# Kernel tuning notes

Hardware: AMD Instinct MI355X
Metric: run time of the kernel (lower is better)

Reference implementation:

```python
import jax, jax.numpy as jnp
import numpy as np

HID = 1024
HEADS = 16
HEAD_DIM = HID // HEADS
FFN = 4096
EPS = 1e-5


def setup_inputs() -> dict:
    key = jax.random.key(0)
    ks = jax.random.split(key, 12)
    s = lambda k, shape, fan_in: jax.random.normal(k, shape, jnp.float32) * (fan_in ** -0.5)
    return {
        "hidden_states": jax.random.normal(ks[0], (2, 2048, HID), jnp.float32),
        "Wq": s(ks[1], (HID, HID), HID),
        "Wk": s(ks[2], (HID, HID), HID),
        "Wv": s(ks[3], (HID, HID), HID),
        "Wo": s(ks[4], (HID, HID), HID),
        "W1": s(ks[5], (HID, FFN), HID),
        "b1": jnp.zeros((FFN,), jnp.float32),
        "W2": s(ks[6], (FFN, HID), FFN),
        "b2": jnp.zeros((HID,), jnp.float32),
        "ln1_scale": jnp.ones((HID,), jnp.float32),
        "ln1_shift": jnp.zeros((HID,), jnp.float32),
        "ln2_scale": jnp.ones((HID,), jnp.float32),
        "ln2_shift": jnp.zeros((HID,), jnp.float32),
    }


def _layer_norm(x, scale, shift):
    mean = jnp.mean(x, axis=-1, keepdims=True)
    var = jnp.var(x, axis=-1, keepdims=True)  # biased, matches unbiased=False
    return (x - mean) * jax.lax.rsqrt(var + EPS) * scale + shift


def _forward(hidden_states, Wq, Wk, Wv, Wo, W1, b1, W2, b2,
             ln1_scale, ln1_shift, ln2_scale, ln2_shift):
    bsz, seq_len, _ = hidden_states.shape
    residual = hidden_states
    x = _layer_norm(hidden_states, ln1_scale, ln1_shift)

    # q/k/v projections -> [b, h, s, d]
    def proj(W):
        return (x @ W).reshape(bsz, seq_len, HEADS, HEAD_DIM).transpose(0, 2, 1, 3)
    q, k, v = proj(Wq), proj(Wk), proj(Wv)

    scores = jnp.einsum("bhqd,bhkd->bhqk", q, k)
    causal = jnp.triu(jnp.ones((seq_len, seq_len), bool), k=1)
    scores = jnp.where(causal, -jnp.inf, scores) / (HEAD_DIM ** 0.5)
    attn = jax.nn.softmax(scores, axis=-1)  # dropout is identity in eval
    out = jnp.einsum("bhqk,bhkd->bhqd", attn, v)
    out = out.transpose(0, 2, 1, 3).reshape(bsz, seq_len, HID)
    hidden_states = residual + out @ Wo

    residual = hidden_states
    y = _layer_norm(hidden_states, ln2_scale, ln2_shift)
    y = jax.nn.gelu(y @ W1 + b1, approximate=False) @ W2 + b2  # torch nn.GELU default = exact erf
    return residual + y


def reference(hidden_states, Wq, Wk, Wv, Wo, W1, b1, W2, b2,
              ln1_scale, ln1_shift, ln2_scale, ln2_shift):
    return _forward(hidden_states, Wq, Wk, Wv, Wo, W1, b1, W2, b2,
                    ln1_scale, ln1_shift, ln2_scale, ln2_shift)
```

## Files before the change

kernel.cpp:

```cpp
#include <hip/hip_runtime.h>
#include <math.h>

using bf16x8 = __attribute__((ext_vector_type(8))) short;
using f32x4  = __attribute__((ext_vector_type(4))) float;

struct __align__(8) us4 { unsigned short x, y, z, w; };
struct __align__(8) u32x2 { unsigned int x, y; };

__device__ __forceinline__ unsigned short f2b(float f) {
  union { float f; unsigned u; } v; v.f = f;
  unsigned r = v.u + 0x7FFFu + ((v.u >> 16) & 1u);
  return (unsigned short)(r >> 16);
}
__device__ __forceinline__ unsigned int cvt_pk_bf16(float lo, float hi) {
  unsigned int d;
  asm("v_cvt_pk_bf16_f32 %0, %1, %2" : "=v"(d) : "v"(lo), "v"(hi));
  return d;
}

#define GLDS(g, l) __builtin_amdgcn_global_load_lds(                        \
    (const __attribute__((address_space(1))) void*)(g),                    \
    (__attribute__((address_space(3))) void*)(l), 16, 0, 0)

__global__ void __launch_bounds__(256) prep_kernel(
    const float* __restrict__ hs, const float* __restrict__ ln1s,
    const float* __restrict__ ln1b, unsigned short* __restrict__ xb,
    const float* __restrict__ Wq, const float* __restrict__ Wk,
    const float* __restrict__ Wv, const float* __restrict__ Wo,
    const float* __restrict__ W1, const float* __restrict__ W2,
    unsigned short* __restrict__ wqkvT, unsigned short* __restrict__ woT,
    unsigned short* __restrict__ w1T, unsigned short* __restrict__ w2T) {
  const int id = blockIdx.x;
  const int t = threadIdx.x;
  __shared__ float tile[32][33];
  __shared__ float red[8];

  if (id < 4096) {
    const int row = id;
    const float4 v = ((const float4*)(hs + (size_t)row * 1024))[t];
    float s  = v.x + v.y + v.z + v.w;
    float s2 = v.x * v.x + v.y * v.y + v.z * v.z + v.w * v.w;
#pragma unroll
    for (int off = 32; off; off >>= 1) {
      s  += __shfl_xor(s,  off);
      s2 += __shfl_xor(s2, off);
    }
    const int w = t >> 6, lane = t & 63;
    if (!lane) { red[w] = s; red[4 + w] = s2; }
    __syncthreads();
    s  = red[0] + red[1] + red[2] + red[3];
    s2 = red[4] + red[5] + red[6] + red[7];
    const float mean = s * (1.0f / 1024.0f);
    const float var  = s2 * (1.0f / 1024.0f) - mean * mean;
    const float rstd = rsqrtf(var + 1e-5f);
    const float4 sc = ((const float4*)ln1s)[t];
    const float4 sh = ((const float4*)ln1b)[t];
    us4 o;
    o.x = f2b((v.x - mean) * rstd * sc.x + sh.x);
    o.y = f2b((v.y - mean) * rstd * sc.y + sh.y);
    o.z = f2b((v.z - mean) * rstd * sc.z + sh.z);
    o.w = f2b((v.w - mean) * rstd * sc.w + sh.w);
    ((us4*)(xb + (size_t)row * 1024))[t] = o;
    return;
  }

  const float* src; unsigned short* dst; int K, N, n0, k0;
  if (id < 8192) {
    const int which = (id - 4096) >> 10, local = (id - 4096) & 1023;
    src = (which == 0) ? Wq : (which == 1) ? Wk : (which == 2) ? Wv : Wo;
    dst = (which == 3) ? woT : wqkvT + (size_t)which * 1048576;
    K = 1024; N = 1024;
    n0 = (local & 31) * 32; k0 = (local >> 5) * 32;
  } else if (id < 12288) {
    const int local = id - 8192;
    src = W1; dst = w1T; K = 1024; N = 4096;
    n0 = (local & 127) * 32; k0 = (local >> 7) * 32;
  } else {
    const int local = id - 12288;
    src = W2; dst = w2T; K = 4096; N = 1024;
    n0 = (local & 31) * 32; k0 = (local >> 5) * 32;
  }
  const int tx = t & 31, ty = t >> 5;
#pragma unroll
  for (int i = 0; i < 32; i += 8)
    tile[ty + i][tx] = src[(size_t)(k0 + ty + i) * N + n0 + tx];
  __syncthreads();
#pragma unroll
  for (int i = 0; i < 32; i += 8)
    dst[(size_t)(n0 + ty + i) * K + k0 + tx] = f2b(tile[tx][ty + i]);
}

__global__ void __launch_bounds__(256) ln_kernel(
    const float* __restrict__ in, const float* __restrict__ scale,
    const float* __restrict__ shift, unsigned short* __restrict__ out) {
  const int row = blockIdx.x, t = threadIdx.x;
  const float4 v = ((const float4*)(in + (size_t)row * 1024))[t];
  float s  = v.x + v.y + v.z + v.w;
  float s2 = v.x * v.x + v.y * v.y + v.z * v.z + v.w * v.w;
#pragma unroll
  for (int off = 32; off; off >>= 1) {
    s  += __shfl_xor(s,  off);
    s2 += __shfl_xor(s2, off);
  }
  __shared__ float red[8];
  const int w = t >> 6, lane = t & 63;
  if (!lane) { red[w] = s; red[4 + w] = s2; }
  __syncthreads();
  s  = red[0] + red[1] + red[2] + red[3];
  s2 = red[4] + red[5] + red[6] + red[7];
  const float mean = s * (1.0f / 1024.0f);
  const float var  = s2 * (1.0f / 1024.0f) - mean * mean;
  const float rstd = rsqrtf(var + 1e-5f);
  const float4 sc = ((const float4*)scale)[t];
  const float4 sh = ((const float4*)shift)[t];
  us4 o;
  o.x = f2b((v.x - mean) * rstd * sc.x + sh.x);
  o.y = f2b((v.y - mean) * rstd * sc.y + sh.y);
  o.z = f2b((v.z - mean) * rstd * sc.z + sh.z);
  o.w = f2b((v.w - mean) * rstd * sc.w + sh.w);
  ((us4*)(out + (size_t)row * 1024))[t] = o;
}

template <int MODE>
__global__ void __launch_bounds__(512, 2) gemm8p(
    const unsigned short* __restrict__ A, const unsigned short* __restrict__ B,
    int K, int N, unsigned short* __restrict__ outb,
    const float* __restrict__ bias, unsigned short* __restrict__ vt) {
  __shared__ unsigned short lA[2][256 * 64];
  __shared__ unsigned short lB[2][256 * 64];
  const int t = threadIdx.x, lane = t & 63;
  const int w = t >> 6, wm = w >> 2, wn = w & 3;
  const int r16 = lane & 15, g = lane >> 4;
  const int m0 = blockIdx.x * 256, n0 = blockIdx.y * 256;

  const unsigned short* aS[2];
  const unsigned short* bS[2];
  int ldst[2];
#pragma unroll
  for (int p = 0; p < 2; ++p) {
    const int ci = t + p * 512, r = ci >> 3, cs = ci & 7;
    aS[p] = A + (size_t)(m0 + r) * K + (cs ^ (r & 7)) * 8;
    bS[p] = B + (size_t)(n0 + r) * K + (cs ^ (r & 7)) * 8;
    ldst[p] = ci * 8;
  }
  const size_t hstep = (size_t)128 * K;

  auto stageA = [&](int buf, int kt, int half) {
    const size_t off = (size_t)kt * 64 + (half ? hstep : 0);
    const int dof = half ? 8192 : 0;
#pragma unroll
    for (int p = 0; p < 2; ++p) GLDS(aS[p] + off, &lA[buf][dof + ldst[p]]);
  };
  auto stageB = [&](int buf, int kt, int half) {
    const size_t off = (size_t)kt * 64 + (half ? hstep : 0);
    const int dof = half ? 8192 : 0;
#pragma unroll
    for (int p = 0; p < 2; ++p) GLDS(bS[p] + off, &lB[buf][dof + ldst[p]]);
  };

  int aOff[8][2], bOff[4][2];
#pragma unroll
  for (int i = 0; i < 8; ++i)
#pragma unroll
    for (int ks = 0; ks < 2; ++ks) {
      const int row = i * 32 + wm * 16 + r16, kb = ks * 4 + g;
      aOff[i][ks] = ((row << 3) + (kb ^ (row & 7))) << 3;
    }
#pragma unroll
  for (int j = 0; j < 4; ++j)
#pragma unroll
    for (int ks = 0; ks < 2; ++ks) {
      const int row = j * 64 + wn * 16 + r16, kb = ks * 4 + g;
      bOff[j][ks] = ((row << 3) + (kb ^ (row & 7))) << 3;
    }

  auto vwait = [](int n) {
    if (n >= 10)     asm volatile("s_waitcnt vmcnt(10)" ::: "memory");
    else if (n >= 8) asm volatile("s_waitcnt vmcnt(8)" ::: "memory");
    else if (n >= 4) asm volatile("s_waitcnt vmcnt(4)" ::: "memory");
    else if (n >= 2) asm volatile("s_waitcnt vmcnt(2)" ::: "memory");
    else             asm volatile("s_waitcnt vmcnt(0)" ::: "memory");
  };

  const int nkt = K >> 6;
  stageA(0, 0, 0); stageB(0, 0, 0); stageB(0, 0, 1); stageA(0, 0, 1);
  stageA(1, 1, 0); stageB(1, 1, 0); stageB(1, 1, 1);
  asm volatile("s_waitcnt vmcnt(10)" ::: "memory");
  __builtin_amdgcn_s_barrier();

  f32x4 acc[8][4] = {};
  bf16x8 af[4][2], b01[2][2], b23[2][2];
  for (int kt = 0; kt < nkt; ++kt) {
    const int cur = kt & 1, nxt = cur ^ 1;
    const unsigned short* bA = lA[cur];
    const unsigned short* bB = lB[cur];
#pragma unroll
    for (int i = 0; i < 4; ++i) {
      af[i][0] = *(const bf16x8*)&bA[aOff[i][0]];
      af[i][1] = *(const bf16x8*)&bA[aOff[i][1]];
    }
#pragma unroll
    for (int j = 0; j < 2; ++j) {
      b01[j][0] = *(const bf16x8*)&bB[bOff[j][0]];
      b01[j][1] = *(const bf16x8*)&bB[bOff[j][1]];
    }
    if (kt + 1 < nkt) stageA(nxt, kt + 1, 1);
    asm volatile("s_waitcnt lgkmcnt(8)" ::: "memory");
    vwait(kt == nkt - 1 ? 2 : 10);
    __builtin_amdgcn_s_barrier();
    asm volatile("s_waitcnt lgkmcnt(0)" ::: "memory");
    __builtin_amdgcn_sched_barrier(0);
    __builtin_amdgcn_s_setprio(1);
#pragma unroll
    for (int i = 0; i < 4; ++i)
#pragma unroll
      for (int j = 0; j < 2; ++j) {
        acc[i][j] = __builtin_amdgcn_mfma_f32_16x16x32_bf16(
            af[i][0], b01[j][0], acc[i][j], 0, 0, 0);
        acc[i][j] = __builtin_amdgcn_mfma_f32_16x16x32_bf16(
            af[i][1], b01[j][1], acc[i][j], 0, 0, 0);
      }
    __builtin_amdgcn_s_setprio(0);
    __builtin_amdgcn_s_barrier();
#pragma unroll
    for (int j = 0; j < 2; ++j) {
      b23[j][0] = *(const bf16x8*)&bB[bOff[2 + j][0]];
      b23[j][1] = *(const bf16x8*)&bB[bOff[2 + j][1]];
    }
    if (kt + 2 < nkt) stageB(cur, kt + 2, 0);
    vwait(kt == nkt - 1 ? 0 : (kt == nkt - 2 ? 8 : 10));
    __builtin_amdgcn_s_barrier();
    asm volatile("s_waitcnt lgkmcnt(0)" ::: "memory");
    __builtin_amdgcn_sched_barrier(0);
    __builtin_amdgcn_s_setprio(1);
#pragma unroll
    for (int i = 0; i < 4; ++i)
#pragma unroll
      for (int j = 0; j < 2; ++j) {
        acc[i][2 + j] = __builtin_amdgcn_mfma_f32_16x16x32_bf16(
            af[i][0], b23[j][0], acc[i][2 + j], 0, 0, 0);
        acc[i][2 + j] = __builtin_amdgcn_mfma_f32_16x16x32_bf16(
            af[i][1], b23[j][1], acc[i][2 + j], 0, 0, 0);
      }
    __builtin_amdgcn_s_setprio(0);
    __builtin_amdgcn_s_barrier();
#pragma unroll
    for (int i = 0; i < 4; ++i) {
      af[i][0] = *(const bf16x8*)&bA[aOff[4 + i][0]];
      af[i][1] = *(const bf16x8*)&bA[aOff[4 + i][1]];
    }
    if (kt + 2 < nkt) stageA(cur, kt + 2, 0);
    __builtin_amdgcn_s_barrier();
    asm volatile("s_waitcnt lgkmcnt(0)" ::: "memory");
    __builtin_amdgcn_sched_barrier(0);
    __builtin_amdgcn_s_setprio(1);
#pragma unroll
    for (int i = 0; i < 4; ++i)
#pragma unroll
      for (int j = 0; j < 2; ++j) {
        acc[4 + i][j] = __builtin_amdgcn_mfma_f32_16x16x32_bf16(
            af[i][0], b01[j][0], acc[4 + i][j], 0, 0, 0);
        acc[4 + i][j] = __builtin_amdgcn_mfma_f32_16x16x32_bf16(
            af[i][1], b01[j][1], acc[4 + i][j], 0, 0, 0);
      }
    __builtin_amdgcn_s_setprio(0);
    __builtin_amdgcn_s_barrier();
    if (kt + 2 < nkt) stageB(cur, kt + 2, 1);
    __builtin_amdgcn_s_barrier();
    __builtin_amdgcn_s_setprio(1);
#pragma unroll
    for (int i = 0; i < 4; ++i)
#pragma unroll
      for (int j = 0; j < 2; ++j) {
        acc[4 + i][2 + j] = __builtin_amdgcn_mfma_f32_16x16x32_bf16(
            af[i][0], b23[j][0], acc[4 + i][2 + j], 0, 0, 0);
        acc[4 + i][2 + j] = __builtin_amdgcn_mfma_f32_16x16x32_bf16(
            af[i][1], b23[j][1], acc[4 + i][2 + j], 0, 0, 0);
      }
    __builtin_amdgcn_s_setprio(0);
    if (kt < nkt - 1) vwait(kt == nkt - 2 ? 4 : 10);
    __builtin_amdgcn_s_barrier();
  }

  float bj[4];
  if constexpr (MODE == 2) {
#pragma unroll
    for (int j = 0; j < 4; ++j)
      bj[j] = bias[n0 + j * 64 + wn * 16 + r16];
  }
#pragma unroll
  for (int i = 0; i < 8; ++i) {
    const int row0 = m0 + i * 32 + wm * 16 + g * 4;
#pragma unroll
    for (int j = 0; j < 4; ++j) {
      const int colb = n0 + j * 64 + wn * 16;
      const int col = colb + r16;
      if constexpr (MODE == 0) {
        if (colb < 2048) {
#pragma unroll
          for (int r = 0; r < 4; ++r)
            outb[(size_t)(row0 + r) * 2048 + col] = f2b(acc[i][j][r]);
        } else {
          const int b = row0 >> 11, s0 = row0 & 2047;
          us4 pk;
          pk.x = f2b(acc[i][j][0]); pk.y = f2b(acc[i][j][1]);
          pk.z = f2b(acc[i][j][2]); pk.w = f2b(acc[i][j][3]);
          *(us4*)&vt[((size_t)b * 1024 + (col - 2048)) * 2048 + s0] = pk;
        }
      } else {
#pragma unroll
        for (int r = 0; r < 4; ++r) {
          const float x = acc[i][j][r] + bj[j];
          const float u = x * (0.7978845608028654f + 0.03567740814f * x * x);
          const float e = __builtin_amdgcn_exp2f(u * 2.885390081777927f);
          const float th = 1.0f - 2.0f * __builtin_amdgcn_rcpf(e + 1.0f);
          outb[(size_t)(row0 + r) * N + col] = f2b(0.5f * x * (1.0f + th));
        }
      }
    }
  }
}

template <int MODE, int BM, int BN>
__global__ void __launch_bounds__(256) gemm_bt(
    const unsigned short* __restrict__ A, const unsigned short* __restrict__ B,
    int K, int N,
    float* __restrict__ outf, const float* __restrict__ bias,
    const float* __restrict__ resid) {
  constexpr int WN = 4;
  constexpr int NJ = BN / (16 * WN);
  constexpr int ACH = BM / 32;
  constexpr int BCH = BN / 32;
  constexpr int TOT = ACH + BCH;
  __shared__ unsigned short lA[2][BM * 64];
  __shared__ unsigned short lB[2][BN * 64];
  const int t = threadIdx.x, lane = t & 63;
  const int w = t >> 6, wm = w / WN, wn = w % WN;
  const int r16 = lane & 15, g = lane >> 4;
  const int m0 = blockIdx.x * BM, n0 = blockIdx.y * BN;

  const unsigned short* aSrc[ACH];
  const unsigned short* bSrc[BCH];
#pragma unroll
  for (int p = 0; p < ACH; ++p) {
    const int ci = t + p * 256, m = ci >> 3, cs = ci & 7;
    aSrc[p] = A + (size_t)(m0 + m) * K + (cs ^ (m & 7)) * 8;
  }
#pragma unroll
  for (int p = 0; p < BCH; ++p) {
    const int ci = t + p * 256, m = ci >> 3, cs = ci & 7;
    bSrc[p] = B + (size_t)(n0 + m) * K + (cs ^ (m & 7)) * 8;
  }

  int aOff[4][2], bOff[NJ][2];
#pragma unroll
  for (int i = 0; i < 4; ++i)
#pragma unroll
    for (int ks = 0; ks < 2; ++ks) {
      const int m = wm * 64 + i * 16 + r16, kb = ks * 4 + g;
      aOff[i][ks] = ((m << 3) + (kb ^ (m & 7))) << 3;
    }
#pragma unroll
  for (int j = 0; j < NJ; ++j)
#pragma unroll
    for (int ks = 0; ks < 2; ++ks) {
      const int n = wn * (16 * NJ) + j * 16 + r16, kb = ks * 4 + g;
      bOff[j][ks] = ((n << 3) + (kb ^ (n & 7))) << 3;
    }

  auto stage = [&](int buf, int kt) {
    const int off = kt * 64;
#pragma unroll
    for (int p = 0; p < ACH; ++p)
      GLDS(aSrc[p] + off, &lA[buf][(t + p * 256) * 8]);
#pragma unroll
    for (int p = 0; p < BCH; ++p)
      GLDS(bSrc[p] + off, &lB[buf][(t + p * 256) * 8]);
  };

  f32x4 acc[4][NJ] = {};
  const int nkt = K >> 6;
  stage(0, 0);
  for (int kt = 0; kt < nkt; ++kt) {
    const int cur = kt & 1;
    if (kt + 1 < nkt) {
      stage(cur ^ 1, kt + 1);
      if constexpr (TOT == 4)
        asm volatile("s_waitcnt vmcnt(4)" ::: "memory");
      else if constexpr (TOT == 6)
        asm volatile("s_waitcnt vmcnt(6)" ::: "memory");
      else
        asm volatile("s_waitcnt vmcnt(8)" ::: "memory");
    } else {
      asm volatile("s_waitcnt vmcnt(0)" ::: "memory");
    }
    __builtin_amdgcn_s_barrier();
    __builtin_amdgcn_sched_barrier(0);
    const unsigned short* bA = lA[cur];
    const unsigned short* bB = lB[cur];
#pragma unroll
    for (int ks = 0; ks < 2; ++ks) {
      bf16x8 af[4], bfr[NJ];
#pragma unroll
      for (int i = 0; i < 4; ++i) af[i] = *(const bf16x8*)&bA[aOff[i][ks]];
#pragma unroll
      for (int j = 0; j < NJ; ++j) bfr[j] = *(const bf16x8*)&bB[bOff[j][ks]];
      __builtin_amdgcn_s_setprio(1);
#pragma unroll
      for (int i = 0; i < 4; ++i)
#pragma unroll
        for (int j = 0; j < NJ; ++j)
          acc[i][j] = __builtin_amdgcn_mfma_f32_16x16x32_bf16(
              af[i], bfr[j], acc[i][j], 0, 0, 0);
      __builtin_amdgcn_s_setprio(0);
    }
    __builtin_amdgcn_sched_barrier(0);
    __builtin_amdgcn_s_barrier();
  }

  float bj[NJ];
  if constexpr (MODE == 3) {
#pragma unroll
    for (int j = 0; j < NJ; ++j)
      bj[j] = bias[n0 + wn * (16 * NJ) + j * 16 + r16];
  }
#pragma unroll
  for (int i = 0; i < 4; ++i) {
    const int row0 = m0 + wm * 64 + i * 16 + g * 4;
#pragma unroll
    for (int j = 0; j < NJ; ++j) {
      const int col = n0 + wn * (16 * NJ) + j * 16 + r16;
      if constexpr (MODE == 1) {
#pragma unroll
        for (int r = 0; r < 4; ++r) {
          const size_t idx = (size_t)(row0 + r) * N + col;
          outf[idx] = acc[i][j][r] + resid[idx];
        }
      } else {
#pragma unroll
        for (int r = 0; r < 4; ++r) {
          const size_t idx = (size_t)(row0 + r) * N + col;
          outf[idx] = acc[i][j][r] + bj[j] + resid[idx];
        }
      }
    }
  }
}

__global__ void __launch_bounds__(256) attn_kernel(
    const unsigned short* __restrict__ qk, const unsigned short* __restrict__ vt,
    unsigned short* __restrict__ obuf) {
  const int j = blockIdx.x, h = blockIdx.y, bb = blockIdx.z;
  const int t = threadIdx.x, lane = t & 63, w = t >> 6;
  const int r16 = lane & 15, g = lane >> 4;
  __shared__ unsigned short lK[2][64 * 64];
  __shared__ unsigned short lV[2][64 * 64];
  __shared__ unsigned short lP[4][16 * 64];

  const int qtA = j, qtB = 31 - j;
  const int ktmax = qtB;
  const int qrowA = qtA * 64 + w * 16 + r16;
  const int qrowB = qtB * 64 + w * 16 + r16;
  const float CE = 0.18033688011112042f;

  bf16x8 qfA[2], qfB[2];
  {
    const unsigned short* qa = qk + (size_t)(bb * 2048 + qrowA) * 2048 + h * 64;
    qfA[0] = *(const bf16x8*)(qa + g * 8);
    qfA[1] = *(const bf16x8*)(qa + 32 + g * 8);
    const unsigned short* qb = qk + (size_t)(bb * 2048 + qrowB) * 2048 + h * 64;
    qfB[0] = *(const bf16x8*)(qb + g * 8);
    qfB[1] = *(const bf16x8*)(qb + 32 + g * 8);
  }

  f32x4 accA[4] = {}, accB[4] = {};
  float mA = -3.0e38f, lA_ = 0.0f, mB = -3.0e38f, lB_ = 0.0f;

  auto stage = [&](int buf, int kt) {
    const int k0 = kt * 64;
#pragma unroll
    for (int p = 0; p < 2; ++p) {
      const int ci = t + p * 256;
      const int r = ci >> 3, cs = ci & 7;
      const int cb = cs ^ (r & 7);
      GLDS(qk + (size_t)(bb * 2048 + k0 + r) * 2048 + 1024 + h * 64 + cb * 8,
           &lK[buf][ci * 8]);
      GLDS(vt + ((size_t)bb * 1024 + h * 64 + r) * 2048 + k0 + cb * 8,
           &lV[buf][ci * 8]);
    }
  };

  const int pswz = (r16 & 7) << 3;

  auto flash_step = [&](const bf16x8* qf, f32x4* accO, float& mrun,
                        float& lrun, int qrow, bool diag, int k0, int cur) {
    f32x4 s[4] = {};
    __builtin_amdgcn_s_setprio(1);
#pragma unroll
    for (int ks = 0; ks < 2; ++ks)
#pragma unroll
      for (int mt = 0; mt < 4; ++mt) {
        const int r = mt * 16 + r16, db = ks * 4 + g;
        const bf16x8 kf =
            *(const bf16x8*)&lK[cur][((r << 3) + (db ^ (r & 7))) << 3];
        s[mt] = __builtin_amdgcn_mfma_f32_16x16x32_bf16(kf, qf[ks], s[mt],
                                                        0, 0, 0);
      }
    __builtin_amdgcn_s_setprio(0);
    if (diag) {
#pragma unroll
      for (int mt = 0; mt < 4; ++mt)
#pragma unroll
        for (int r = 0; r < 4; ++r)
          if (k0 + mt * 16 + g * 4 + r > qrow) s[mt][r] = -3.0e38f;
    }
    float tmax = -3.0e38f;
#pragma unroll
    for (int mt = 0; mt < 4; ++mt)
#pragma unroll
      for (int r = 0; r < 4; ++r) tmax = fmaxf(tmax, s[mt][r]);
    tmax = fmaxf(tmax, __shfl_xor(tmax, 16));
    tmax = fmaxf(tmax, __shfl_xor(tmax, 32));
    if (!__all(tmax <= mrun + 44.0f)) {
      const float mnew = fmaxf(mrun, tmax);
      const float fac = __builtin_amdgcn_exp2f((mrun - mnew) * CE);
      lrun *= fac;
      float fr[4];
#pragma unroll
      for (int r = 0; r < 4; ++r) fr[r] = __shfl(fac, g * 4 + r);
#pragma unroll
      for (int nb = 0; nb < 4; ++nb)
#pragma unroll
        for (int r = 0; r < 4; ++r) accO[nb][r] *= fr[r];
      mrun = mnew;
    }
    float pv[4][4];
    float tsum = 0.0f;
#pragma unroll
    for (int mt = 0; mt < 4; ++mt)
#pragma unroll
      for (int r = 0; r < 4; ++r) {
        pv[mt][r] = __builtin_amdgcn_exp2f((s[mt][r] - mrun) * CE);
        tsum += pv[mt][r];
      }
    tsum += __shfl_xor(tsum, 16);
    tsum += __shfl_xor(tsum, 32);
    lrun += tsum;
#pragma unroll
    for (int mt = 0; mt < 4; ++mt) {
      u32x2 pk;
      pk.x = cvt_pk_bf16(pv[mt][0], pv[mt][1]);
      pk.y = cvt_pk_bf16(pv[mt][2], pv[mt][3]);
      *(u32x2*)&lP[w][r16 * 64 + ((mt * 16 + g * 4) ^ pswz)] = pk;
    }
    __builtin_amdgcn_s_setprio(1);
#pragma unroll
    for (int ks = 0; ks < 2; ++ks) {
      const bf16x8 pa =
          *(const bf16x8*)&lP[w][r16 * 64 + ((ks * 32 + g * 8) ^ pswz)];
#pragma unroll
      for (int nb = 0; nb < 4; ++nb) {
        const int d = nb * 16 + r16, kb = ks * 4 + g;
        const bf16x8 vf =
            *(const bf16x8*)&lV[cur][((d << 3) + (kb ^ (d & 7))) << 3];
        accO[nb] = __builtin_amdgcn_mfma_f32_16x16x32_bf16(pa, vf, accO[nb],
                                                           0, 0, 0);
      }
    }
    __builtin_amdgcn_s_setprio(0);
  };

  stage(0, 0);
  __syncthreads();
  int cur = 0;
  for (int kt = 0; kt <= ktmax; ++kt) {
    if (kt < ktmax) stage(cur ^ 1, kt + 1);
    flash_step(qfB, accB, mB, lB_, qrowB, kt == qtB, kt * 64, cur);
    if (kt <= qtA)
      flash_step(qfA, accA, mA, lA_, qrowA, kt == qtA, kt * 64, cur);
    __syncthreads();
    cur ^= 1;
  }

  auto epilogue = [&](const f32x4* accO, float lrun, int q0) {
    const float li = 1.0f / lrun;
    float lr_[4];
#pragma unroll
    for (int r = 0; r < 4; ++r) lr_[r] = __shfl(li, g * 4 + r);
#pragma unroll
    for (int nb = 0; nb < 4; ++nb)
#pragma unroll
      for (int r = 0; r < 4; ++r) {
        const int row = bb * 2048 + q0 + w * 16 + g * 4 + r;
        const int col = h * 64 + nb * 16 + r16;
        obuf[(size_t)row * 1024 + col] = f2b(accO[nb][r] * lr_[r]);
      }
  };
  epilogue(accA, lA_, qtA * 64);
  epilogue(accB, lB_, qtB * 64);
}

extern "C" void kernel_launch(void* const* d_in, const int* in_sizes, int n_in,
                              void* d_out, int out_size, void* d_ws,
                              size_t ws_size, hipStream_t stream) {
  const float* hs   = (const float*)d_in[0];
  const float* Wq   = (const float*)d_in[1];
  const float* Wk   = (const float*)d_in[2];
  const float* Wv   = (const float*)d_in[3];
  const float* Wo   = (const float*)d_in[4];
  const float* W1   = (const float*)d_in[5];
  const float* b1   = (const float*)d_in[6];
  const float* W2   = (const float*)d_in[7];
  const float* b2   = (const float*)d_in[8];
  const float* ln1s = (const float*)d_in[9];
  const float* ln1b = (const float*)d_in[10];
  const float* ln2s = (const float*)d_in[11];
  const float* ln2b = (const float*)d_in[12];
  float* out = (float*)d_out;

  char* ws = (char*)d_ws;
  unsigned short* wqkvT = (unsigned short*)(ws + 0);
  unsigned short* woT   = (unsigned short*)(ws + 6291456);
  unsigned short* w1T   = (unsigned short*)(ws + 8388608);
  unsigned short* w2T   = (unsigned short*)(ws + 16777216);
  float*          hid   = (float*)(ws + 25165824);
  unsigned short* xb    = (unsigned short*)(ws + 41943040);
  char*           big   = ws + 50331648;
  unsigned short* qkb   = (unsigned short*)(big);
  unsigned short* vtb   = (unsigned short*)(big + 16777216);
  unsigned short* ob    = (unsigned short*)(big + 25165824);
  unsigned short* h1    = (unsigned short*)(big);

  prep_kernel<<<16384, 256, 0, stream>>>(hs, ln1s, ln1b, xb,
                                         Wq, Wk, Wv, Wo, W1, W2,
                                         wqkvT, woT, w1T, w2T);
  gemm8p<0><<<dim3(16, 12), 512, 0, stream>>>(xb, wqkvT, 1024, 3072,
                                              qkb, nullptr, vtb);
  attn_kernel<<<dim3(16, 16, 2), 256, 0, stream>>>(qkb, vtb, ob);
  gemm_bt<1, 64, 64><<<dim3(64, 16), 256, 0, stream>>>(ob, woT, 1024, 1024,
                                                       hid, nullptr, hs);
  ln_kernel<<<4096, 256, 0, stream>>>(hid, ln2s, ln2b, xb);
  gemm8p<2><<<dim3(16, 16), 512, 0, stream>>>(xb, w1T, 1024, 4096,
                                              h1, b1, nullptr);
  gemm_bt<3, 64, 64><<<dim3(64, 16), 256, 0, stream>>>(h1, w2T, 4096, 1024,
                                                       out, b2, hid);
}
```

Measured before the change: 219.3 us.

## Interleave QK MFMAs for both query tiles and overlap softmax with PV

Result: no change. 222.6 us (+1.5%).

```diff
diff --git a/kernel.cpp b/kernel.cpp
--- a/kernel.cpp
+++ b/kernel.cpp
@@ -455,7 +455,7 @@
   const int r16 = lane & 15, g = lane >> 4;
   __shared__ unsigned short lK[2][64 * 64];
   __shared__ unsigned short lV[2][64 * 64];
-  __shared__ unsigned short lP[4][16 * 64];
+  __shared__ unsigned short lP[4][2][16 * 64];
 
   const int qtA = j, qtB = 31 - j;
   const int ktmax = qtB;
@@ -492,21 +492,8 @@
 
   const int pswz = (r16 & 7) << 3;
 
-  auto flash_step = [&](const bf16x8* qf, f32x4* accO, float& mrun,
-                        float& lrun, int qrow, bool diag, int k0, int cur) {
-    f32x4 s[4] = {};
-    __builtin_amdgcn_s_setprio(1);
-#pragma unroll
-    for (int ks = 0; ks < 2; ++ks)
-#pragma unroll
-      for (int mt = 0; mt < 4; ++mt) {
-        const int r = mt * 16 + r16, db = ks * 4 + g;
-        const bf16x8 kf =
-            *(const bf16x8*)&lK[cur][((r << 3) + (db ^ (r & 7))) << 3];
-        s[mt] = __builtin_amdgcn_mfma_f32_16x16x32_bf16(kf, qf[ks], s[mt],
-                                                        0, 0, 0);
-      }
-    __builtin_amdgcn_s_setprio(0);
+  auto softmax_pk = [&](f32x4* s, f32x4* accO, float& mrun, float& lrun,
+                        int qrow, bool diag, int k0, u32x2* pk) {
     if (diag) {
 #pragma unroll
       for (int mt = 0; mt < 4; ++mt)
@@ -534,30 +521,34 @@
         for (int r = 0; r < 4; ++r) accO[nb][r] *= fr[r];
       mrun = mnew;
     }
-    float pv[4][4];
     float tsum = 0.0f;
 #pragma unroll
-    for (int mt = 0; mt < 4; ++mt)
-#pragma unroll
-      for (int r = 0; r < 4; ++r) {
-        pv[mt][r] = __builtin_amdgcn_exp2f((s[mt][r] - mrun) * CE);
-        tsum += pv[mt][r];
-      }
+    for (int mt = 0; mt < 4; ++mt) {
+      float p0 = __builtin_amdgcn_exp2f((s[mt][0] - mrun) * CE);
+      float p1 = __builtin_amdgcn_exp2f((s[mt][1] - mrun) * CE);
+      float p2 = __builtin_amdgcn_exp2f((s[mt][2] - mrun) * CE);
+      float p3 = __builtin_amdgcn_exp2f((s[mt][3] - mrun) * CE);
+      tsum += (p0 + p1) + (p2 + p3);
+      pk[mt].x = cvt_pk_bf16(p0, p1);
+      pk[mt].y = cvt_pk_bf16(p2, p3);
+    }
     tsum += __shfl_xor(tsum, 16);
     tsum += __shfl_xor(tsum, 32);
     lrun += tsum;
-#pragma unroll
-    for (int mt = 0; mt < 4; ++mt) {
-      u32x2 pk;
-      pk.x = cvt_pk_bf16(pv[mt][0], pv[mt][1]);
-      pk.y = cvt_pk_bf16(pv[mt][2], pv[mt][3]);
-      *(u32x2*)&lP[w][r16 * 64 + ((mt * 16 + g * 4) ^ pswz)] = pk;
-    }
+  };
+
+  auto write_pk = [&](const u32x2* pk, int tile) {
+#pragma unroll
+    for (int mt = 0; mt < 4; ++mt)
+      *(u32x2*)&lP[w][tile][r16 * 64 + ((mt * 16 + g * 4) ^ pswz)] = pk[mt];
+  };
+
+  auto pv_mfma = [&](f32x4* accO, int tile, int cur) {
     __builtin_amdgcn_s_setprio(1);
 #pragma unroll
     for (int ks = 0; ks < 2; ++ks) {
       const bf16x8 pa =
-          *(const bf16x8*)&lP[w][r16 * 64 + ((ks * 32 + g * 8) ^ pswz)];
+          *(const bf16x8*)&lP[w][tile][r16 * 64 + ((ks * 32 + g * 8) ^ pswz)];
 #pragma unroll
       for (int nb = 0; nb < 4; ++nb) {
         const int d = nb * 16 + r16, kb = ks * 4 + g;
@@ -574,10 +565,50 @@
   __syncthreads();
   int cur = 0;
   for (int kt = 0; kt <= ktmax; ++kt) {
+    const int k0 = kt * 64;
     if (kt < ktmax) stage(cur ^ 1, kt + 1);
-    flash_step(qfB, accB, mB, lB_, qrowB, kt == qtB, kt * 64, cur);
-    if (kt <= qtA)
-      flash_step(qfA, accA, mA, lA_, qrowA, kt == qtA, kt * 64, cur);
+    if (kt <= qtA) {
+      f32x4 sB[4] = {}, sA[4] = {};
+      __builtin_amdgcn_s_setprio(1);
+#pragma unroll
+      for (int ks = 0; ks < 2; ++ks)
+#pragma unroll
+        for (int mt = 0; mt < 4; ++mt) {
+          const int r = mt * 16 + r16, db = ks * 4 + g;
+          const bf16x8 kf =
+              *(const bf16x8*)&lK[cur][((r << 3) + (db ^ (r & 7))) << 3];
+          sB[mt] = __builtin_amdgcn_mfma_f32_16x16x32_bf16(kf, qfB[ks],
+                                                           sB[mt], 0, 0, 0);
+          sA[mt] = __builtin_amdgcn_mfma_f32_16x16x32_bf16(kf, qfA[ks],
+                                                           sA[mt], 0, 0, 0);
+        }
+      __builtin_amdgcn_s_setprio(0);
+      u32x2 pkB[4], pkA[4];
+      softmax_pk(sB, accB, mB, lB_, qrowB, kt == qtB, k0, pkB);
+      write_pk(pkB, 0);
+      softmax_pk(sA, accA, mA, lA_, qrowA, kt == qtA, k0, pkA);
+      pv_mfma(accB, 0, cur);
+      write_pk(pkA, 1);
+      pv_mfma(accA, 1, cur);
+    } else {
+      f32x4 sB[4] = {};
+      __builtin_amdgcn_s_setprio(1);
+#pragma unroll
+      for (int ks = 0; ks < 2; ++ks)
+#pragma unroll
+        for (int mt = 0; mt < 4; ++mt) {
+          const int r = mt * 16 + r16, db = ks * 4 + g;
+          const bf16x8 kf =
+              *(const bf16x8*)&lK[cur][((r << 3) + (db ^ (r & 7))) << 3];
+          sB[mt] = __builtin_amdgcn_mfma_f32_16x16x32_bf16(kf, qfB[ks],
+                                                           sB[mt], 0, 0, 0);
+        }
+      __builtin_amdgcn_s_setprio(0);
+      u32x2 pkB[4];
+      softmax_pk(sB, accB, mB, lB_, qrowB, kt == qtB, k0, pkB);
+      write_pk(pkB, 0);
+      pv_mfma(accB, 0, cur);
+    }
     __syncthreads();
     cur ^= 1;
   }
```

## Split-K the FFN down-projection over big-tile GEMM with separate reduce kernel

Applied to the files above, without the earlier changes.

After: 218.5 us. About the same (-0.4%).

```diff
diff --git a/kernel.cpp b/kernel.cpp
--- a/kernel.cpp
+++ b/kernel.cpp
@@ -11,6 +11,10 @@
   union { float f; unsigned u; } v; v.f = f;
   unsigned r = v.u + 0x7FFFu + ((v.u >> 16) & 1u);
   return (unsigned short)(r >> 16);
+}
+__device__ __forceinline__ float b2f(unsigned short b) {
+  union { unsigned u; float f; } v; v.u = ((unsigned)b) << 16;
+  return v.f;
 }
 __device__ __forceinline__ unsigned int cvt_pk_bf16(float lo, float hi) {
   unsigned int d;
@@ -121,17 +125,45 @@
   ((us4*)(out + (size_t)row * 1024))[t] = o;
 }
 
+__global__ void __launch_bounds__(256) ffn_reduce(
+    const unsigned short* __restrict__ p0, const unsigned short* __restrict__ p1,
+    const unsigned short* __restrict__ p2, const unsigned short* __restrict__ p3,
+    const float* __restrict__ bias, const float* __restrict__ resid,
+    float* __restrict__ out) {
+  const int row = blockIdx.x, t = threadIdx.x;
+  const size_t idx = (size_t)row * 1024 + t * 4;
+  const us4 a0 = *(const us4*)&p0[idx];
+  const us4 a1 = *(const us4*)&p1[idx];
+  const us4 a2 = *(const us4*)&p2[idx];
+  const us4 a3 = *(const us4*)&p3[idx];
+  const float4 bb = ((const float4*)bias)[t];
+  const float4 rr = ((const float4*)(resid + (size_t)row * 1024))[t];
+  float4 o;
+  o.x = (b2f(a0.x) + b2f(a1.x)) + (b2f(a2.x) + b2f(a3.x)) + bb.x + rr.x;
+  o.y = (b2f(a0.y) + b2f(a1.y)) + (b2f(a2.y) + b2f(a3.y)) + bb.y + rr.y;
+  o.z = (b2f(a0.z) + b2f(a1.z)) + (b2f(a2.z) + b2f(a3.z)) + bb.z + rr.z;
+  o.w = (b2f(a0.w) + b2f(a1.w)) + (b2f(a2.w) + b2f(a3.w)) + bb.w + rr.w;
+  ((float4*)(out + (size_t)row * 1024))[t] = o;
+}
+
 template <int MODE>
 __global__ void __launch_bounds__(512, 2) gemm8p(
     const unsigned short* __restrict__ A, const unsigned short* __restrict__ B,
     int K, int N, unsigned short* __restrict__ outb,
-    const float* __restrict__ bias, unsigned short* __restrict__ vt) {
+    const float* __restrict__ bias, unsigned short* __restrict__ vt,
+    unsigned short* __restrict__ o1, unsigned short* __restrict__ o2,
+    unsigned short* __restrict__ o3, int nkt_) {
   __shared__ unsigned short lA[2][256 * 64];
   __shared__ unsigned short lB[2][256 * 64];
   const int t = threadIdx.x, lane = t & 63;
   const int w = t >> 6, wm = w >> 2, wn = w & 3;
   const int r16 = lane & 15, g = lane >> 4;
   const int m0 = blockIdx.x * 256, n0 = blockIdx.y * 256;
+  const int z = blockIdx.z;
+  const int kb = z * nkt_;
+  unsigned short* outp = outb;
+  if constexpr (MODE == 4)
+    outp = (z == 0) ? outb : (z == 1) ? o1 : (z == 2) ? o2 : o3;
 
   const unsigned short* aS[2];
   const unsigned short* bS[2];
@@ -146,13 +178,13 @@
   const size_t hstep = (size_t)128 * K;
 
   auto stageA = [&](int buf, int kt, int half) {
-    const size_t off = (size_t)kt * 64 + (half ? hstep : 0);
+    const size_t off = (size_t)(kb + kt) * 64 + (half ? hstep : 0);
     const int dof = half ? 8192 : 0;
 #pragma unroll
     for (int p = 0; p < 2; ++p) GLDS(aS[p] + off, &lA[buf][dof + ldst[p]]);
   };
   auto stageB = [&](int buf, int kt, int half) {
-    const size_t off = (size_t)kt * 64 + (half ? hstep : 0);
+    const size_t off = (size_t)(kb + kt) * 64 + (half ? hstep : 0);
     const int dof = half ? 8192 : 0;
 #pragma unroll
     for (int p = 0; p < 2; ++p) GLDS(bS[p] + off, &lB[buf][dof + ldst[p]]);
@@ -163,15 +195,15 @@
   for (int i = 0; i < 8; ++i)
 #pragma unroll
     for (int ks = 0; ks < 2; ++ks) {
-      const int row = i * 32 + wm * 16 + r16, kb = ks * 4 + g;
-      aOff[i][ks] = ((row << 3) + (kb ^ (row & 7))) << 3;
+      const int row = i * 32 + wm * 16 + r16, kk = ks * 4 + g;
+      aOff[i][ks] = ((row << 3) + (kk ^ (row & 7))) << 3;
     }
 #pragma unroll
   for (int j = 0; j < 4; ++j)
 #pragma unroll
     for (int ks = 0; ks < 2; ++ks) {
-      const int row = j * 64 + wn * 16 + r16, kb = ks * 4 + g;
-      bOff[j][ks] = ((row << 3) + (kb ^ (row & 7))) << 3;
+      const int row = j * 64 + wn * 16 + r16, kk = ks * 4 + g;
+      bOff[j][ks] = ((row << 3) + (kk ^ (row & 7))) << 3;
     }
 
   auto vwait = [](int n) {
@@ -182,7 +214,7 @@
     else             asm volatile("s_waitcnt vmcnt(0)" ::: "memory");
   };
 
-  const int nkt = K >> 6;
+  const int nkt = nkt_;
   stageA(0, 0, 0); stageB(0, 0, 0); stageB(0, 0, 1); stageA(0, 0, 1);
   stageA(1, 1, 0); stageB(1, 1, 0); stageB(1, 1, 1);
   asm volatile("s_waitcnt vmcnt(10)" ::: "memory");
@@ -307,7 +339,7 @@
           pk.z = f2b(acc[i][j][2]); pk.w = f2b(acc[i][j][3]);
           *(us4*)&vt[((size_t)b * 1024 + (col - 2048)) * 2048 + s0] = pk;
         }
-      } else {
+      } else if constexpr (MODE == 2) {
 #pragma unroll
         for (int r = 0; r < 4; ++r) {
           const float x = acc[i][j][r] + bj[j];
@@ -316,6 +348,10 @@
           const float th = 1.0f - 2.0f * __builtin_amdgcn_rcpf(e + 1.0f);
           outb[(size_t)(row0 + r) * N + col] = f2b(0.5f * x * (1.0f + th));
         }
+      } else {
+#pragma unroll
+        for (int r = 0; r < 4; ++r)
+          outp[(size_t)(row0 + r) * N + col] = f2b(acc[i][j][r]);
       }
     }
   }
@@ -418,30 +454,16 @@
     __builtin_amdgcn_s_barrier();
   }
 
-  float bj[NJ];
-  if constexpr (MODE == 3) {
-#pragma unroll
-    for (int j = 0; j < NJ; ++j)
-      bj[j] = bias[n0 + wn * (16 * NJ) + j * 16 + r16];
-  }
 #pragma unroll
   for (int i = 0; i < 4; ++i) {
     const int row0 = m0 + wm * 64 + i * 16 + g * 4;
 #pragma unroll
     for (int j = 0; j < NJ; ++j) {
       const int col = n0 + wn * (16 * NJ) + j * 16 + r16;
-      if constexpr (MODE == 1) {
-#pragma unroll
-        for (int r = 0; r < 4; ++r) {
-          const size_t idx = (size_t)(row0 + r) * N + col;
-          outf[idx] = acc[i][j][r] + resid[idx];
-        }
-      } else {
-#pragma unroll
-        for (int r = 0; r < 4; ++r) {
-          const size_t idx = (size_t)(row0 + r) * N + col;
-          outf[idx] = acc[i][j][r] + bj[j] + resid[idx];
-        }
+#pragma unroll
+      for (int r = 0; r < 4; ++r) {
+        const size_t idx = (size_t)(row0 + r) * N + col;
+        outf[idx] = acc[i][j][r] + resid[idx];
       }
     }
   }
@@ -630,18 +652,26 @@
   unsigned short* vtb   = (unsigned short*)(big + 16777216);
   unsigned short* ob    = (unsigned short*)(big + 25165824);
   unsigned short* h1    = (unsigned short*)(big);
+  unsigned short* sp0 = (unsigned short*)(ws + 0);
+  unsigned short* sp1 = (unsigned short*)(ws + 8388608);
+  unsigned short* sp2 = (unsigned short*)(ws + 41943040);
+  unsigned short* sp3 = (unsigned short*)(ws + 83886080);
 
   prep_kernel<<<16384, 256, 0, stream>>>(hs, ln1s, ln1b, xb,
                                          Wq, Wk, Wv, Wo, W1, W2,
                                          wqkvT, woT, w1T, w2T);
   gemm8p<0><<<dim3(16, 12), 512, 0, stream>>>(xb, wqkvT, 1024, 3072,
-                                              qkb, nullptr, vtb);
+                                              qkb, nullptr, vtb,
+                                              nullptr, nullptr, nullptr, 16);
   attn_kernel<<<dim3(16, 16, 2), 256, 0, stream>>>(qkb, vtb, ob);
   gemm_bt<1, 64, 64><<<dim3(64, 16), 256, 0, stream>>>(ob, woT, 1024, 1024,
                                                        hid, nullptr, hs);
   ln_kernel<<<4096, 256, 0, stream>>>(hid, ln2s, ln2b, xb);
   gemm8p<2><<<dim3(16, 16), 512, 0, stream>>>(xb, w1T, 1024, 4096,
-                                              h1, b1, nullptr);
-  gemm_bt<3, 64, 64><<<dim3(64, 16), 256, 0, stream>>>(h1, w2T, 4096, 1024,
-                                                       out, b2, hid);
-}
+                                              h1, b1, nullptr,
+                                              nullptr, nullptr, nullptr, 16);
+  gemm8p<4><<<dim3(16, 4, 4), 512, 0, stream>>>(h1, w2T, 4096, 1024,
+                                                sp0, nullptr, nullptr,
+                                                sp1, sp2, sp3, 16);
+  ffn_reduce<<<4096, 256, 0, stream>>>(sp0, sp1, sp2, sp3, b2, hid, out);
+}
```
